# Kernel tuning notes

Measured on AMD Instinct MI355X. Metric: run time of the kernel, lower is better.

Reference implementation:

```python
import jax, jax.numpy as jnp
import numpy as np

B, S, H = 4, 2048, 2048
N_HEADS, KV_HEADS, RANK = 16, 8, 64
HEAD_DIM = H // N_HEADS          # 128
N_REP = N_HEADS // KV_HEADS      # 2
NEG = -1e9


def setup_inputs() -> dict:
    key = jax.random.key(0)
    ks = jax.random.split(key, 6)
    hidden_states = jax.random.normal(ks[0], (B, S, H), dtype=jnp.float32)
    # additive causal mask, broadcast over heads: [B,1,S,S]
    causal = jnp.tril(jnp.ones((S, S), dtype=bool))
    attention_mask = jnp.where(causal, 0.0, NEG).astype(jnp.float32)
    attention_mask = jnp.broadcast_to(attention_mask[None, None], (B, 1, S, S))
    sc = 1.0 / np.sqrt(H)
    Wq = jax.random.normal(ks[1], (H, RANK), dtype=jnp.float32) * sc
    Wk = jax.random.normal(ks[2], (H, RANK), dtype=jnp.float32) * sc
    Wv = jax.random.normal(ks[3], (H, KV_HEADS * HEAD_DIM), dtype=jnp.float32) * sc
    Wo = jax.random.normal(ks[4], (H, H), dtype=jnp.float32) * sc
    return {"hidden_states": hidden_states, "attention_mask": attention_mask,
            "Wq": Wq, "Wk": Wk, "Wv": Wv, "Wo": Wo}


def reference(hidden_states, attention_mask, Wq, Wk, Wv, Wo):
    b, s, h = hidden_states.shape
    # low-rank CP factors shared across heads: [B,S,R]
    q = hidden_states @ Wq
    k = hidden_states @ Wk
    # values with GQA: [B, kv_heads, S, head_dim] -> repeat to [B, n_heads, S, head_dim]
    v = (hidden_states @ Wv).reshape(b, s, KV_HEADS, HEAD_DIM).transpose(0, 2, 1, 3)
    v = jnp.repeat(v, N_REP, axis=1)
    # CP circuit over the (i,j) grid: scores[b,i,j] = sum_r q[b,i,r] * k[b,j,r]
    # (Hadamard over embedding factors gathered at grid indices, SumLayer with unit
    #  weights over rank; the all-ones head factor multiplies by 1). Head-shared.
    scores = jnp.einsum('bir,bjr->bij', q, k)[:, None]  # [B,1,S,S]
    scores = scores + attention_mask                     # additive causal mask
    probs = jax.nn.softmax(scores.astype(jnp.float32), axis=-1).astype(v.dtype)
    # attn_probs @ V, broadcasting the head-shared probs over heads
    ctx = jnp.einsum('bij,bhjd->bhid', probs[:, 0], v)   # [B,H,S,D]
    ctx = ctx.transpose(0, 2, 1, 3).reshape(b, s, h)
    return ctx @ Wo
```

## Files before the change

### kernel.cpp

```cpp
#include <hip/hip_runtime.h>

#define B_ 4
#define S_ 2048
#define H_ 2048
#define R_ 64
#define DKV_ 1024

typedef __attribute__((ext_vector_type(8))) short s16x8;
typedef __attribute__((ext_vector_type(4))) float f32x4v;

__device__ __forceinline__ unsigned short f2bf(float x) {
  unsigned int u = __builtin_bit_cast(unsigned int, x);
  u += 0x7FFF + ((u >> 16) & 1);
  return (unsigned short)(u >> 16);
}
__device__ __forceinline__ float bf2f(unsigned short h) {
  unsigned int u = ((unsigned int)h) << 16;
  return __builtin_bit_cast(float, u);
}

__device__ __forceinline__ void gl_lds16(const void* g, void* l) {
  __builtin_amdgcn_global_load_lds(
      (const __attribute__((address_space(1))) unsigned int*)g,
      (__attribute__((address_space(3))) unsigned int*)l, 16, 0, 0);
}

__device__ __forceinline__ int swz_off(int m, int kb) {
  int L = m >> 1;
  int slot = ((m & 1) << 2) | (kb >> 4);
  int sp = slot ^ (L & 7);
  return (L << 7) | (sp << 4) | (kb & 15);
}

__global__ __launch_bounds__(256) void k_transpose_bf16(const float* __restrict__ in,
    unsigned short* __restrict__ out, int rows, int cols) {
  __shared__ float tile[32][33];
  int c0 = blockIdx.x * 32, r0 = blockIdx.y * 32;
  int tx = threadIdx.x & 31, ty = threadIdx.x >> 5;
  for (int i = 0; i < 4; ++i)
    tile[ty + i * 8][tx] = in[(size_t)(r0 + ty + i * 8) * cols + c0 + tx];
  __syncthreads();
  for (int i = 0; i < 4; ++i)
    out[(size_t)(c0 + ty + i * 8) * rows + r0 + tx] = f2bf(tile[tx][ty + i * 8]);
}

__global__ __launch_bounds__(256) void k_build_wqkt(const float* __restrict__ Wq,
    const float* __restrict__ Wk, unsigned short* __restrict__ hiT,
    unsigned short* __restrict__ loT) {
  __shared__ float tile[32][33];
  int k0 = blockIdx.x * 32, n0 = blockIdx.y * 32;
  const float* W = (n0 < 64) ? Wq : Wk;
  int nb = n0 & 63;
  int tx = threadIdx.x & 31, ty = threadIdx.x >> 5;
  for (int i = 0; i < 4; ++i)
    tile[ty + i * 8][tx] = W[(size_t)(k0 + ty + i * 8) * R_ + nb + tx];
  __syncthreads();
  for (int i = 0; i < 4; ++i) {
    float v = tile[tx][ty + i * 8];
    unsigned short h = f2bf(v);
    size_t idx = (size_t)(n0 + ty + i * 8) * H_ + k0 + tx;
    hiT[idx] = h;
    loT[idx] = f2bf(v - bf2f(h));
  }
}

__global__ __launch_bounds__(256) void k_build_wot(const float* __restrict__ Wo,
                                                   unsigned short* __restrict__ WoT) {
  __shared__ float tile[32][33];
  int n0 = blockIdx.x * 32, r0 = blockIdx.y * 32;
  int h1b = 256 * (r0 >> 7) + (r0 & 127);
  int tx = threadIdx.x & 31, ty = threadIdx.x >> 5;
  for (int i = 0; i < 4; ++i) {
    int dr = ty + i * 8;
    tile[dr][tx] = Wo[(size_t)(h1b + dr) * H_ + n0 + tx] +
                   Wo[(size_t)(h1b + 128 + dr) * H_ + n0 + tx];
  }
  __syncthreads();
  for (int i = 0; i < 4; ++i)
    WoT[(size_t)(n0 + ty + i * 8) * DKV_ + r0 + tx] = f2bf(tile[tx][ty + i * 8]);
}

__global__ __launch_bounds__(512, 8) void k_qk_split(
    const float* __restrict__ hs,
    const unsigned short* __restrict__ Bhi, const unsigned short* __restrict__ Blo,
    unsigned short* __restrict__ hsb, float* __restrict__ part) {
  constexpr int TQK = 20480;
  __shared__ __attribute__((aligned(16))) char lds[2 * TQK];
  int m0 = blockIdx.x * 32;
  int kc0 = blockIdx.y * 512;
  int t = threadIdx.x;
  int lane = t & 63, wave = t >> 6;
  int lr = lane & 15, kb = (lane >> 4) << 4;

  int arow = t >> 4;
  const float* asrc = hs + (size_t)(m0 + arow) * H_ + kc0 + ((t & 15) << 1);
  unsigned short* hdst = hsb + (size_t)(m0 + arow) * H_ + kc0 + ((t & 15) << 1);
  int adst = swz_off(arow, (t & 15) << 2);

  auto stageB = [&](int kt, char* base) {
    int k0 = kc0 + (kt << 5);
    int L = t >> 3;
    int slot = (t & 7) ^ (L & 7);
    int n = (L << 1) | (slot >> 2);
    int ke = (slot & 3) << 3;
    gl_lds16(Bhi + (size_t)n * H_ + k0 + ke, base + 4096 + t * 16);
    gl_lds16(Blo + (size_t)n * H_ + k0 + ke, base + 12288 + t * 16);
  };

  auto convA = [&](const float2& v, char* wbuf, int kt) {
    ushort2 h, l;
    h.x = f2bf(v.x); h.y = f2bf(v.y);
    l.x = f2bf(v.x - bf2f(h.x)); l.y = f2bf(v.y - bf2f(h.y));
    *(ushort2*)(wbuf + adst) = h;
    *(ushort2*)(wbuf + 2048 + adst) = l;
    *(ushort2*)(hdst + (size_t)kt * 32) = h;
  };

  float2 R0 = *(const float2*)(asrc);
  stageB(0, &lds[0]);
  float2 Rcur = *(const float2*)(asrc + 32);
  asm volatile("s_waitcnt vmcnt(3)" ::: "memory");
  convA(R0, &lds[0], 0);

  f32x4v acc[2] = {};
  for (int kt = 0; kt < 16; ++kt) {
    char* curb = &lds[(kt & 1) * TQK];
    char* nxtb = &lds[((kt + 1) & 1) * TQK];
    if (kt + 1 < 16) stageB(kt + 1, nxtb);
    float2 Rnext;
    if (kt + 2 < 16) Rnext = *(const float2*)(asrc + (size_t)(kt + 2) * 32);
    __builtin_amdgcn_sched_barrier(0);
    if (kt + 2 < 16) asm volatile("s_waitcnt vmcnt(4) lgkmcnt(0)" ::: "memory");
    else if (kt + 1 < 16) asm volatile("s_waitcnt vmcnt(3) lgkmcnt(0)" ::: "memory");
    else asm volatile("s_waitcnt vmcnt(0) lgkmcnt(0)" ::: "memory");
    __builtin_amdgcn_s_barrier();
    __builtin_amdgcn_sched_barrier(0);
    if (kt + 1 < 16) convA(Rcur, nxtb, kt + 1);
    Rcur = Rnext;
    s16x8 ah[2], al[2], bh, bl;
#pragma unroll
    for (int m = 0; m < 2; ++m) {
      int o = swz_off(m * 16 + lr, kb);
      ah[m] = *(const s16x8*)(curb + o);
      al[m] = *(const s16x8*)(curb + 2048 + o);
    }
    {
      int o = swz_off(wave * 16 + lr, kb);
      bh = *(const s16x8*)(curb + 4096 + o);
      bl = *(const s16x8*)(curb + 12288 + o);
    }
    __builtin_amdgcn_s_setprio(1);
#pragma unroll
    for (int m = 0; m < 2; ++m) {
      acc[m] = __builtin_amdgcn_mfma_f32_16x16x32_bf16(ah[m], bh, acc[m], 0, 0, 0);
      acc[m] = __builtin_amdgcn_mfma_f32_16x16x32_bf16(ah[m], bl, acc[m], 0, 0, 0);
      acc[m] = __builtin_amdgcn_mfma_f32_16x16x32_bf16(al[m], bh, acc[m], 0, 0, 0);
    }
    __builtin_amdgcn_s_setprio(0);
  }

  float* Pp = part + (size_t)blockIdx.y * (8192 * 128);
#pragma unroll
  for (int m = 0; m < 2; ++m) {
    int lrow = m * 16 + ((lane >> 4) << 2);
    int lcol = wave * 16 + lr;
#pragma unroll
    for (int r = 0; r < 4; ++r)
      Pp[(size_t)(m0 + lrow + r) * 128 + lcol] = acc[m][r];
  }
}

__global__ __launch_bounds__(256) void k_qk_reduce(const float* __restrict__ part,
    unsigned short* __restrict__ qkh, unsigned short* __restrict__ qkl) {
  constexpr size_t CH = (size_t)8192 * 128;
  size_t i = ((size_t)blockIdx.x * 256 + threadIdx.x) * 4;
  float4 a = *(const float4*)(part + i);
  float4 b = *(const float4*)(part + CH + i);
  float4 c = *(const float4*)(part + 2 * CH + i);
  float4 d = *(const float4*)(part + 3 * CH + i);
  float v[4] = {a.x + b.x + c.x + d.x, a.y + b.y + c.y + d.y,
                a.z + b.z + c.z + d.z, a.w + b.w + c.w + d.w};
  ushort4 h, l;
  unsigned short* hp = (unsigned short*)&h;
  unsigned short* lp = (unsigned short*)&l;
#pragma unroll
  for (int r = 0; r < 4; ++r) {
    hp[r] = f2bf(v[r]);
    lp[r] = f2bf(v[r] - bf2f(hp[r]));
  }
  *(ushort4*)(qkh + i) = h;
  *(ushort4*)(qkl + i) = l;
}

__global__ __launch_bounds__(512, 4) void k_attn_fused(
    const unsigned short* __restrict__ qkh, const unsigned short* __restrict__ qkl,
    const unsigned short* __restrict__ VT, unsigned short* __restrict__ ctx) {
  constexpr int TILEB = 24576;
  __shared__ __attribute__((aligned(16))) char lds[3 * TILEB + 4096 + 256];
  char* Pt = &lds[3 * TILEB];
  float* rs = (float*)&lds[3 * TILEB + 4096];

  int t = threadIdx.x;
  int gx = gridDim.x;
  int x = blockIdx.x;
  int bx = (x & 1) ? (gx - 1 - (x >> 1)) : (x >> 1);
  if (blockIdx.z & 2) bx = gx - 1 - bx;
  int z = blockIdx.z;
  int m0 = bx * 64, d0 = blockIdx.y * 256;

  int lane = t & 63, wave = t >> 6;
  int sm = wave >> 1, sn = wave & 1;
  int wr = wave >> 2, wc = wave & 3;
  int kb = (lane >> 4) << 4;

  const unsigned short* qh = qkh + (size_t)z * S_ * 128;
  const unsigned short* ql = qkl + (size_t)z * S_ * 128;

  s16x8 qfh[2], qfl[2];
  {
    size_t rq = (size_t)(m0 + sm * 16 + (lane & 15)) * 128 + ((lane >> 4) << 3);
    qfh[0] = *(const s16x8*)(qh + rq);
    qfh[1] = *(const s16x8*)(qh + rq + 32);
    qfl[0] = *(const s16x8*)(ql + rq);
    qfl[1] = *(const s16x8*)(ql + rq + 32);
  }

  auto stage = [&](int kt, int buf) {
    int j0 = kt << 5;
    char* base = &lds[buf * TILEB];
    {
      int q = t & 127;
      int L = q >> 3;
      int slot = (q & 7) ^ (L & 7);
      int jr = (L << 1) | (slot >> 2);
      int ke = (slot & 3) << 3;
      int sub = t >> 7;
      const unsigned short* src = ((sub < 2) ? qh : ql) +
          (size_t)(j0 + jr) * 128 + 64 + ((sub & 1) << 5) + ke;
      gl_lds16(src, base + sub * 2048 + q * 16);
    }
    char* vb = base + 8192;
#pragma unroll
    for (int c = 0; c < 2; ++c) {
      int q = c * 512 + t;
      int L = q >> 3;
      int slot = (q & 7) ^ (L & 7);
      int dr = (L << 1) | (slot >> 2);
      int ke = (slot & 3) << 3;
      gl_lds16(VT + (size_t)(d0 + dr) * (B_ * S_) + (size_t)z * S_ + j0 + ke,
               vb + q * 16);
    }
  };

  if (t < 64) rs[t] = 0.f;
  int NT = (m0 + 64) >> 5;
  stage(0, 0);
  stage(1, 1);

  int jrow = sn * 16 + (lane & 15);
  int koffs = swz_off(jrow, kb);
  int paoff[2], voff[4];
#pragma unroll
  for (int mf = 0; mf < 2; ++mf)
    paoff[mf] = swz_off(wr * 32 + mf * 16 + (lane & 15), kb);
#pragma unroll
  for (int nf = 0; nf < 4; ++nf)
    voff[nf] = swz_off(wc * 64 + nf * 16 + (lane & 15), kb);

  float ps[4] = {0.f, 0.f, 0.f, 0.f};
  f32x4v accp[2][4] = {};
  int prow = sm * 16 + ((lane >> 4) << 2);
  int pcol = sn * 16 + (lane & 15);

  int cur = 0, nxt = 2;
  for (int kt = 0; kt < NT; ++kt) {
    __builtin_amdgcn_sched_barrier(0);
    if (kt + 1 < NT) asm volatile("s_waitcnt vmcnt(3) lgkmcnt(0)" ::: "memory");
    else asm volatile("s_waitcnt vmcnt(0) lgkmcnt(0)" ::: "memory");
    __builtin_amdgcn_s_barrier();
    __builtin_amdgcn_sched_barrier(0);
    if (kt + 2 < NT) stage(kt + 2, nxt);
    const char* base = &lds[cur * TILEB];
    s16x8 kh[2], kl[2];
    kh[0] = *(const s16x8*)(base + koffs);
    kh[1] = *(const s16x8*)(base + 2048 + koffs);
    kl[0] = *(const s16x8*)(base + 4096 + koffs);
    kl[1] = *(const s16x8*)(base + 6144 + koffs);
    f32x4v s = {};
#pragma unroll
    for (int ks = 0; ks < 2; ++ks) {
      s = __builtin_amdgcn_mfma_f32_16x16x32_bf16(qfh[ks], kh[ks], s, 0, 0, 0);
      s = __builtin_amdgcn_mfma_f32_16x16x32_bf16(qfh[ks], kl[ks], s, 0, 0, 0);
      s = __builtin_amdgcn_mfma_f32_16x16x32_bf16(qfl[ks], kh[ks], s, 0, 0, 0);
    }
    int jg = (kt << 5) + pcol;
    int ig = m0 + prow;
#pragma unroll
    for (int r = 0; r < 4; ++r) {
      float p = (jg <= ig + r) ? __expf(s[r]) : 0.f;
      ps[r] += p;
      *(unsigned short*)(Pt + swz_off(prow + r, pcol * 2)) = f2bf(p);
    }
    __builtin_amdgcn_sched_barrier(0);
    asm volatile("s_waitcnt lgkmcnt(0)" ::: "memory");
    __builtin_amdgcn_s_barrier();
    __builtin_amdgcn_sched_barrier(0);
    s16x8 pa[2], vf[4];
#pragma unroll
    for (int mf = 0; mf < 2; ++mf) pa[mf] = *(const s16x8*)(Pt + paoff[mf]);
    const char* vbase = base + 8192;
#pragma unroll
    for (int nf = 0; nf < 4; ++nf) vf[nf] = *(const s16x8*)(vbase + voff[nf]);
    __builtin_amdgcn_s_setprio(1);
#pragma unroll
    for (int mf = 0; mf < 2; ++mf)
#pragma unroll
      for (int nf = 0; nf < 4; ++nf)
        accp[mf][nf] =
            __builtin_amdgcn_mfma_f32_16x16x32_bf16(pa[mf], vf[nf], accp[mf][nf], 0, 0, 0);
    __builtin_amdgcn_s_setprio(0);
    cur = (cur == 2) ? 0 : cur + 1;
    nxt = (nxt == 2) ? 0 : nxt + 1;
  }

#pragma unroll
  for (int r = 0; r < 4; ++r) {
    float v = ps[r];
    for (int msk = 1; msk < 16; msk <<= 1) v += __shfl_xor(v, msk, 64);
    if ((lane & 15) == 0) atomicAdd(&rs[prow + r], v);
  }
  __syncthreads();

  unsigned short* Cp = ctx + (size_t)(z * S_ + m0) * DKV_ + d0;
#pragma unroll
  for (int mf = 0; mf < 2; ++mf) {
    int lr0 = wr * 32 + mf * 16 + ((lane >> 4) << 2);
#pragma unroll
    for (int nf = 0; nf < 4; ++nf) {
      int lc = wc * 64 + nf * 16 + (lane & 15);
#pragma unroll
      for (int r = 0; r < 4; ++r) {
        float sc = 1.f / rs[lr0 + r];
        Cp[(size_t)(lr0 + r) * DKV_ + lc] = f2bf(accp[mf][nf][r] * sc);
      }
    }
  }
}

template <int BM, int BN, bool TRANS_OUT, bool OUT_BF16>
__global__ __launch_bounds__(512, 4) void k_gemm256(
    const unsigned short* __restrict__ A, int lda,
    const unsigned short* __restrict__ BT, int ldbt,
    void* __restrict__ C, int ldc, int K) {
  constexpr int ABYTES = BM * 64;
  constexpr int BBYTES = BN * 64;
  constexpr int TILEB = ABYTES + BBYTES;
  constexpr int WARPS_M = 4;
  constexpr int WARPS_N = 2;
  constexpr int WM = BM / WARPS_M;
  constexpr int WN = BN / WARPS_N;
  constexpr int MF = WM / 16;
  constexpr int NF = WN / 16;
  constexpr int LPS = BM / 128 + BN / 128;
  __shared__ __attribute__((aligned(16))) char lds[3 * TILEB];

  int t = threadIdx.x;
  int gx = gridDim.x;
  int id = blockIdx.y * gx + blockIdx.x;
  int cpx = gx >> 3;
  int xcd = id & 7, rr = id >> 3;
  int bx = xcd * cpx + rr % cpx;
  int by = rr / cpx;
  int m0 = bx * BM, n0 = by * BN;

  const unsigned short* Ab = A + (size_t)m0 * lda;
  const unsigned short* Bb = BT + (size_t)n0 * ldbt;

  int lane = t & 63, wave = t >> 6;
  int wr = wave / WARPS_N, wc = wave % WARPS_N;
  int kb = (lane >> 4) << 4;
  int aoff[MF], boff[NF];
#pragma unroll
  for (int mf = 0; mf < MF; ++mf)
    aoff[mf] = swz_off(wr * WM + mf * 16 + (lane & 15), kb);
#pragma unroll
  for (int nf = 0; nf < NF; ++nf)
    boff[nf] = swz_off(wc * WN + nf * 16 + (lane & 15), kb);

  int NT = K >> 5;

  auto stage = [&](int kt, int buf) {
    int k0 = kt << 5;
    char* la = &lds[buf * TILEB];
    char* lb = la + ABYTES;
#pragma unroll
    for (int c = 0; c < BM / 128; ++c) {
      int q = c * 512 + t;
      int L = q >> 3;
      int slot = (q & 7) ^ (L & 7);
      int m = (L << 1) | (slot >> 2);
      int ke = (slot & 3) << 3;
      gl_lds16(Ab + (size_t)m * lda + k0 + ke, la + q * 16);
    }
#pragma unroll
    for (int c = 0; c < BN / 128; ++c) {
      int q = c * 512 + t;
      int L = q >> 3;
      int slot = (q & 7) ^ (L & 7);
      int n = (L << 1) | (slot >> 2);
      int ke = (slot & 3) << 3;
      gl_lds16(Bb + (size_t)n * ldbt + k0 + ke, lb + q * 16);
    }
  };

  f32x4v acc[MF][NF] = {};
  stage(0, 0);
  if (NT > 1) stage(1, 1);
  int cur = 0, nxt = 2;
  for (int kt = 0; kt < NT; ++kt) {
    __builtin_amdgcn_sched_barrier(0);
    if (kt + 1 < NT) {
      if constexpr (LPS == 2) asm volatile("s_waitcnt vmcnt(2)" ::: "memory");
      else asm volatile("s_waitcnt vmcnt(3)" ::: "memory");
    } else {
      asm volatile("s_waitcnt vmcnt(0)" ::: "memory");
    }
    __builtin_amdgcn_s_barrier();
    __builtin_amdgcn_sched_barrier(0);
    if (kt + 2 < NT) stage(kt + 2, nxt);
    const char* la = &lds[cur * TILEB];
    const char* lb = la + ABYTES;
    s16x8 af[MF], bf[NF];
#pragma unroll
    for (int mf = 0; mf < MF; ++mf) af[mf] = *(const s16x8*)(la + aoff[mf]);
#pragma unroll
    for (int nf = 0; nf < NF; ++nf) bf[nf] = *(const s16x8*)(lb + boff[nf]);
    __builtin_amdgcn_s_setprio(1);
#pragma unroll
    for (int mf = 0; mf < MF; ++mf)
#pragma unroll
      for (int nf = 0; nf < NF; ++nf)
        acc[mf][nf] =
            __builtin_amdgcn_mfma_f32_16x16x32_bf16(af[mf], bf[nf], acc[mf][nf], 0, 0, 0);
    __builtin_amdgcn_s_setprio(0);
    cur = (cur == 2) ? 0 : cur + 1;
    nxt = (nxt == 2) ? 0 : nxt + 1;
  }

#pragma unroll
  for (int mf = 0; mf < MF; ++mf) {
    int lrow = wr * WM + mf * 16 + ((lane >> 4) << 2);
#pragma unroll
    for (int nf = 0; nf < NF; ++nf) {
      int lcol = wc * WN + nf * 16 + (lane & 15);
      f32x4v v = acc[mf][nf];
      if (TRANS_OUT) {
        ushort4 o;
        o.x = f2bf(v[0]); o.y = f2bf(v[1]); o.z = f2bf(v[2]); o.w = f2bf(v[3]);
        unsigned short* Cp = (unsigned short*)C;
        *(ushort4*)&Cp[(size_t)(n0 + lcol) * ldc + m0 + lrow] = o;
      } else {
#pragma unroll
        for (int r = 0; r < 4; ++r) {
          if (OUT_BF16) {
            unsigned short* Cp = (unsigned short*)C;
            Cp[(size_t)(m0 + lrow + r) * ldc + n0 + lcol] = f2bf(v[r]);
          } else {
            float* Cp = (float*)C;
            Cp[(size_t)(m0 + lrow + r) * ldc + n0 + lcol] = v[r];
          }
        }
      }
    }
  }
}

extern "C" void kernel_launch(void* const* d_in, const int* in_sizes, int n_in,
                              void* d_out, int out_size, void* d_ws, size_t ws_size,
                              hipStream_t stream) {
  const float* hs = (const float*)d_in[0];
  const float* Wq = (const float*)d_in[2];
  const float* Wk = (const float*)d_in[3];
  const float* Wv = (const float*)d_in[4];
  const float* Wo = (const float*)d_in[5];
  float* out = (float*)d_out;

  char* w = (char*)d_ws;
  unsigned short* hsb = (unsigned short*)w; w += (size_t)B_ * S_ * H_ * 2;
  unsigned short* WvT = (unsigned short*)w; w += (size_t)DKV_ * H_ * 2;
  unsigned short* WoT = (unsigned short*)w; w += (size_t)H_ * DKV_ * 2;
  unsigned short* WqkTh = (unsigned short*)w; w += (size_t)128 * H_ * 2;
  unsigned short* WqkTl = (unsigned short*)w; w += (size_t)128 * H_ * 2;
  unsigned short* VT  = (unsigned short*)w; w += (size_t)DKV_ * B_ * S_ * 2;
  unsigned short* ctx = (unsigned short*)w; w += (size_t)B_ * S_ * DKV_ * 2;
  unsigned short* qkh = (unsigned short*)w; w += (size_t)B_ * S_ * 128 * 2;
  unsigned short* qkl = (unsigned short*)w; w += (size_t)B_ * S_ * 128 * 2;
  float* part = (float*)w; w += (size_t)4 * B_ * S_ * 128 * 4;

  k_transpose_bf16<<<dim3(DKV_ / 32, H_ / 32), 256, 0, stream>>>(Wv, WvT, H_, DKV_);
  k_build_wot<<<dim3(H_ / 32, DKV_ / 32), 256, 0, stream>>>(Wo, WoT);
  k_build_wqkt<<<dim3(H_ / 32, 4), 256, 0, stream>>>(Wq, Wk, WqkTh, WqkTl);
  k_qk_split<<<dim3(B_ * S_ / 32, 4), 512, 0, stream>>>(hs, WqkTh, WqkTl, hsb, part);
  k_qk_reduce<<<(B_ * S_ * 128) / (256 * 4), 256, 0, stream>>>(part, qkh, qkl);
  k_gemm256<256, 128, true, true>
      <<<dim3(B_ * S_ / 256, DKV_ / 128), 512, 0, stream>>>(
      hsb, H_, WvT, H_, VT, B_ * S_, H_);
  k_attn_fused<<<dim3(32, 4, B_), 512, 0, stream>>>(qkh, qkl, VT, ctx);
  k_gemm256<256, 128, false, false>
      <<<dim3(B_ * S_ / 256, H_ / 128), 512, 0, stream>>>(
      ctx, DKV_, WoT, DKV_, out, H_, DKV_);
}
```

Before: 189.1 us.

## Triple-buffer LDS and deepen prefetch pipeline in QK split GEMM

Changes the k_qk_split main loop from double to triple LDS buffering. B tiles are now staged two iterations ahead and A rows are held in a three-slot register ring. The loop is fully unrolled with hand-placed waitcnt counts. LDS use grows by half and the occupancy hint in launch_bounds drops from 8 to 4, trading occupancy for more latency hiding. The hand-tuned vmcnt values must match the new load order exactly, so the ordering is fragile.

```diff
diff --git a/kernel.cpp b/kernel.cpp
--- a/kernel.cpp
+++ b/kernel.cpp
@@ -80,12 +80,13 @@
     WoT[(size_t)(n0 + ty + i * 8) * DKV_ + r0 + tx] = f2bf(tile[tx][ty + i * 8]);
 }
 
-__global__ __launch_bounds__(512, 8) void k_qk_split(
+__global__ __launch_bounds__(512, 4) void k_qk_split(
     const float* __restrict__ hs,
     const unsigned short* __restrict__ Bhi, const unsigned short* __restrict__ Blo,
     unsigned short* __restrict__ hsb, float* __restrict__ part) {
   constexpr int TQK = 20480;
-  __shared__ __attribute__((aligned(16))) char lds[2 * TQK];
+  constexpr int NT = 16;
+  __shared__ __attribute__((aligned(16))) char lds[3 * TQK];
   int m0 = blockIdx.x * 32;
   int kc0 = blockIdx.y * 512;
   int t = threadIdx.x;
@@ -116,27 +117,40 @@
     *(ushort2*)(hdst + (size_t)kt * 32) = h;
   };
 
-  float2 R0 = *(const float2*)(asrc);
+  float2 Rring[3];
+  Rring[0] = *(const float2*)(asrc);
+  Rring[1] = *(const float2*)(asrc + 32);
   stageB(0, &lds[0]);
-  float2 Rcur = *(const float2*)(asrc + 32);
-  asm volatile("s_waitcnt vmcnt(3)" ::: "memory");
-  convA(R0, &lds[0], 0);
+  stageB(1, &lds[TQK]);
+  __builtin_amdgcn_sched_barrier(0);
+  asm volatile("s_waitcnt vmcnt(4)" ::: "memory");
+  __builtin_amdgcn_sched_barrier(0);
+  convA(Rring[0], &lds[0], 0);
 
   f32x4v acc[2] = {};
-  for (int kt = 0; kt < 16; ++kt) {
-    char* curb = &lds[(kt & 1) * TQK];
-    char* nxtb = &lds[((kt + 1) & 1) * TQK];
-    if (kt + 1 < 16) stageB(kt + 1, nxtb);
-    float2 Rnext;
-    if (kt + 2 < 16) Rnext = *(const float2*)(asrc + (size_t)(kt + 2) * 32);
-    __builtin_amdgcn_sched_barrier(0);
-    if (kt + 2 < 16) asm volatile("s_waitcnt vmcnt(4) lgkmcnt(0)" ::: "memory");
-    else if (kt + 1 < 16) asm volatile("s_waitcnt vmcnt(3) lgkmcnt(0)" ::: "memory");
-    else asm volatile("s_waitcnt vmcnt(0) lgkmcnt(0)" ::: "memory");
+#pragma unroll
+  for (int kt = 0; kt < NT; ++kt) {
+    char* curb = &lds[(kt % 3) * TQK];
+    char* nb1 = &lds[((kt + 1) % 3) * TQK];
+    char* nb2 = &lds[((kt + 2) % 3) * TQK];
+    __builtin_amdgcn_sched_barrier(0);
+    if (kt == 0 || kt == NT - 1)
+      asm volatile("s_waitcnt vmcnt(1) lgkmcnt(0)" ::: "memory");
+    else
+      asm volatile("s_waitcnt vmcnt(4) lgkmcnt(0)" ::: "memory");
+    __builtin_amdgcn_sched_barrier(0);
     __builtin_amdgcn_s_barrier();
     __builtin_amdgcn_sched_barrier(0);
-    if (kt + 1 < 16) convA(Rcur, nxtb, kt + 1);
-    Rcur = Rnext;
+    if (kt + 2 < NT)
+      Rring[(kt + 2) % 3] = *(const float2*)(asrc + (size_t)(kt + 2) * 32);
+    if (kt + 1 < NT) {
+      __builtin_amdgcn_sched_barrier(0);
+      if (kt + 2 < NT) asm volatile("s_waitcnt vmcnt(4)" ::: "memory");
+      else asm volatile("s_waitcnt vmcnt(3)" ::: "memory");
+      __builtin_amdgcn_sched_barrier(0);
+      convA(Rring[(kt + 1) % 3], nb1, kt + 1);
+      if (kt + 2 < NT) stageB(kt + 2, nb2);
+    }
     s16x8 ah[2], al[2], bh, bl;
 #pragma unroll
     for (int m = 0; m < 2; ++m) {
```

Result: slower. 200.4 us (median of 4 runs) (+5.9%).
